# Optimization experiments

Hardware: AMD Instinct MI355X
Metric: run time of the kernel (lower is better)

The kernel has to match this reference:

```python
import jax, jax.numpy as jnp
import numpy as np

N_NODES = 50000
NNZ = 1_600_000
D_FEAT = 256


def setup_inputs() -> dict:
    key = jax.random.key(0)
    k_x, k_v, k_r, k_c = jax.random.split(key, 4)
    x = jax.random.normal(k_x, (N_NODES, D_FEAT), dtype=jnp.float32)
    # learned per-nonzero values; torch init uses std = 1/sqrt(mean col degree)
    std = 1.0 / np.sqrt(NNZ / N_NODES)
    values = jax.random.normal(k_v, (NNZ,), dtype=jnp.float32) * std
    row = jax.random.randint(k_r, (NNZ,), 0, N_NODES, dtype=jnp.int64)
    col = jax.random.randint(k_c, (NNZ,), 0, N_NODES, dtype=jnp.int64)
    return {"x": x, "values": values, "row": row, "col": col}


def reference(x, values, row, col):
    # Math identical to matmul(to_dense(coo(row, col, values)), x):
    # out[r] = sum over edges e with row[e]==r of values[e] * x[col[e]]
    msgs = values[:, None] * x[col]            # [nnz, F]
    out = jax.ops.segment_sum(msgs, row, num_segments=N_NODES)  # [N, F]
    return out
```

## Files before the change

kernel.cpp:

```cpp
#include <hip/hip_runtime.h>
#include <hip/hip_bf16.h>


#define FEAT 256
#define CAP 128
#define SCAN_CHUNK 2048

static __device__ __forceinline__ unsigned short f2bf(float f) {
    unsigned int u = __float_as_uint(f);
    u += 0x7FFF + ((u >> 16) & 1);
    return (unsigned short)(u >> 16);
}
static __device__ __forceinline__ float bf2f(unsigned short h) {
    return __uint_as_float(((unsigned int)h) << 16);
}


__global__ __launch_bounds__(256) void zero_convx_kernel(const float4* __restrict__ x4,
                                                         ushort4* __restrict__ xh,
                                                         int* __restrict__ deg,
                                                         int n, int n4) {
    const int stride = gridDim.x * blockDim.x;
    const int tid = blockIdx.x * blockDim.x + threadIdx.x;
    for (int i = tid; i < n; i += stride) deg[i] = 0;
    for (int i = tid; i < n4; i += stride) {
        float4 v = x4[i];
        ushort4 o;
        o.x = f2bf(v.x); o.y = f2bf(v.y); o.z = f2bf(v.z); o.w = f2bf(v.w);
        xh[i] = o;
    }
}

__global__ __launch_bounds__(256) void bucket_scatter_kernel(const int* __restrict__ row,
                                                             const int* __restrict__ col,
                                                             const float* __restrict__ vals,
                                                             int* __restrict__ deg,
                                                             int2* __restrict__ pack,
                                                             int nnz) {
    const int stride = gridDim.x * blockDim.x;
    for (int e = blockIdx.x * blockDim.x + threadIdx.x; e < nnz; e += stride) {
        int r = row[e];
        int pos = atomicAdd(&deg[r], 1);
        if (pos < CAP) pack[(size_t)r * CAP + pos] = make_int2(col[e], __float_as_int(vals[e]));
    }
}

__global__ __launch_bounds__(256) void spmm_bucket_kernel(const ushort4* __restrict__ xh,
                                                          const int2* __restrict__ pack,
                                                          const int* __restrict__ deg,
                                                          float* __restrict__ out, int n) {
    const int wave = threadIdx.x >> 6;
    const int lane = threadIdx.x & 63;
    const int r = blockIdx.x * 4 + wave;
    if (r >= n) return;
    int d = deg[r]; if (d > CAP) d = CAP;
    const int2* __restrict__ bucket = pack + (size_t)r * CAP;
    float4 acc = make_float4(0.f, 0.f, 0.f, 0.f);
    for (int k0 = 0; k0 < d; k0 += 64) {
        int cnt = d - k0; if (cnt > 64) cnt = 64;
        float myv = 0.f; int myc = 0;
        if (lane < cnt) {
            int2 pr = bucket[k0 + lane];
            myc = pr.x;
            myv = __int_as_float(pr.y);
        }
        for (int j = 0; j < cnt; ++j) {
            float v = __shfl(myv, j);
            int   c = __shfl(myc, j);
            ushort4 h = xh[c * 64 + lane];
            acc.x += v * bf2f(h.x);
            acc.y += v * bf2f(h.y);
            acc.z += v * bf2f(h.z);
            acc.w += v * bf2f(h.w);
        }
    }
    ((float4*)out)[r * 64 + lane] = acc;
}


__global__ void convx_kernel(const float4* __restrict__ x, ushort4* __restrict__ xh, int n4) {
    int stride = gridDim.x * blockDim.x;
    for (int i = blockIdx.x * blockDim.x + threadIdx.x; i < n4; i += stride) {
        float4 v = x[i];
        ushort4 o;
        o.x = f2bf(v.x); o.y = f2bf(v.y); o.z = f2bf(v.z); o.w = f2bf(v.w);
        xh[i] = o;
    }
}

__global__ void hist_rank_kernel(const int* __restrict__ row, int* __restrict__ deg,
                                 int* __restrict__ rank, int nnz) {
    int stride = gridDim.x * blockDim.x;
    for (int e = blockIdx.x * blockDim.x + threadIdx.x; e < nnz; e += stride) {
        rank[e] = atomicAdd(&deg[row[e]], 1);
    }
}

__global__ __launch_bounds__(256) void scan_chunks_kernel(const int* __restrict__ deg,
                                                          int* __restrict__ rowstart,
                                                          int* __restrict__ partials, int n) {
    __shared__ int s[256];
    const int tid = threadIdx.x;
    const int base = blockIdx.x * SCAN_CHUNK + tid * 8;
    int items[8];
    int sum = 0;
    #pragma unroll
    for (int j = 0; j < 8; ++j) {
        int v = (base + j < n) ? deg[base + j] : 0;
        items[j] = sum;
        sum += v;
    }
    s[tid] = sum;
    __syncthreads();
    for (int off = 1; off < 256; off <<= 1) {
        int t = (tid >= off) ? s[tid - off] : 0;
        __syncthreads();
        s[tid] += t;
        __syncthreads();
    }
    int thread_prefix = s[tid] - sum;
    if (tid == 255) partials[blockIdx.x] = s[255];
    #pragma unroll
    for (int j = 0; j < 8; ++j) {
        if (base + j < n) rowstart[base + j] = items[j] + thread_prefix;
    }
}

__global__ __launch_bounds__(256) void finalize_scan_kernel(int* __restrict__ rowstart,
                                                            const int* __restrict__ partials,
                                                            int n, int nnz) {
    __shared__ int sprefix;
    const int cb = (int)((blockIdx.x * 256u) / SCAN_CHUNK);
    if (threadIdx.x < 64) {
        int v = (threadIdx.x < cb) ? partials[threadIdx.x] : 0;
        #pragma unroll
        for (int off = 32; off; off >>= 1) v += __shfl_down(v, off);
        if (threadIdx.x == 0) sprefix = v;
    }
    __syncthreads();
    int i = blockIdx.x * 256 + threadIdx.x;
    if (i < n) rowstart[i] += sprefix;
    if (i == 0) rowstart[n] = nnz;
}

__global__ void scatter_pack_kernel(const int* __restrict__ row, const int* __restrict__ rank,
                                    const int* __restrict__ col, const float* __restrict__ vals,
                                    const int* __restrict__ rowstart, int2* __restrict__ pack,
                                    int nnz) {
    int stride = gridDim.x * blockDim.x;
    for (int e = blockIdx.x * blockDim.x + threadIdx.x; e < nnz; e += stride) {
        int p = rowstart[row[e]] + rank[e];
        pack[p] = make_int2(col[e], __float_as_int(vals[e]));
    }
}

__global__ __launch_bounds__(256) void spmm_bf16_kernel(const ushort4* __restrict__ xh,
                                                        const int2* __restrict__ pack,
                                                        const int* __restrict__ rowstart,
                                                        float* __restrict__ out, int n) {
    const int wave = threadIdx.x >> 6;
    const int lane = threadIdx.x & 63;
    const int r = blockIdx.x * 4 + wave;
    if (r >= n) return;
    const int s = rowstart[r];
    const int e = rowstart[r + 1];
    float4 acc = make_float4(0.f, 0.f, 0.f, 0.f);
    for (int k0 = s; k0 < e; k0 += 64) {
        int cnt = e - k0; if (cnt > 64) cnt = 64;
        float myv = 0.f; int myc = 0;
        if (lane < cnt) {
            int2 pr = pack[k0 + lane];
            myc = pr.x;
            myv = __int_as_float(pr.y);
        }
        for (int j = 0; j < cnt; ++j) {
            float v = __shfl(myv, j);
            int   c = __shfl(myc, j);
            ushort4 h = xh[c * 64 + lane];
            acc.x += v * bf2f(h.x);
            acc.y += v * bf2f(h.y);
            acc.z += v * bf2f(h.z);
            acc.w += v * bf2f(h.w);
        }
    }
    ((float4*)out)[r * 64 + lane] = acc;
}


extern "C" void kernel_launch(void* const* d_in, const int* in_sizes, int n_in,
                              void* d_out, int out_size, void* d_ws, size_t ws_size,
                              hipStream_t stream) {
    const float* x    = (const float*)d_in[0];
    const float* vals = (const float*)d_in[1];
    const int*   row  = (const int*)d_in[2];
    const int*   col  = (const int*)d_in[3];
    float* out = (float*)d_out;

    const int nnz = in_sizes[1];
    const int n   = out_size / FEAT;
    const int nb  = (n + SCAN_CHUNK - 1) / SCAN_CHUNK;

    {
        char* p0 = (char*)d_ws;
        char* p = p0;
        int* deg = (int*)p;            p += (size_t)n * 4;
        p = (char*)((((size_t)p) + 15) & ~(size_t)15);
        int2* pack = (int2*)p;         p += (size_t)n * CAP * 8;
        ushort4* xh = (ushort4*)p;     p += (size_t)n * FEAT * 2;
        const size_t need = (size_t)(p - p0);
        if (ws_size >= need) {
            const int n4 = n * (FEAT / 4);
            zero_convx_kernel<<<2048, 256, 0, stream>>>((const float4*)x, xh, deg, n, n4);
            bucket_scatter_kernel<<<2048, 256, 0, stream>>>(row, col, vals, deg, pack, nnz);
            spmm_bucket_kernel<<<(n + 3) / 4, 256, 0, stream>>>(xh, pack, deg, out, n);
            return;
        }
    }

    {
        char* p0 = (char*)d_ws;
        char* p = p0;
        int* deg      = (int*)p; p += (size_t)n * 4;
        int* rowstart = (int*)p; p += (size_t)(n + 1) * 4;
        int* partials = (int*)p; p += 64 * 4;
        int* rank     = (int*)p; p += (size_t)nnz * 4;
        p = (char*)((((size_t)p) + 7) & ~(size_t)7);
        int2* pack    = (int2*)p; p += (size_t)nnz * 8;
        unsigned short* xh = (unsigned short*)p; p += (size_t)n * FEAT * 2;
        const size_t need = (size_t)(p - p0);
        if (ws_size >= need) {
            hipMemsetAsync(deg, 0, (size_t)n * 4, stream);
            hist_rank_kernel<<<2048, 256, 0, stream>>>(row, deg, rank, nnz);
            convx_kernel<<<2048, 256, 0, stream>>>((const float4*)x, (ushort4*)xh, n * (FEAT / 4));
            scan_chunks_kernel<<<nb, 256, 0, stream>>>(deg, rowstart, partials, n);
            finalize_scan_kernel<<<(n + 255) / 256, 256, 0, stream>>>(rowstart, partials, n, nnz);
            scatter_pack_kernel<<<2048, 256, 0, stream>>>(row, rank, col, vals, rowstart, pack, nnz);
            spmm_bf16_kernel<<<(n + 3) / 4, 256, 0, stream>>>((const ushort4*)xh, pack, rowstart, out, n);
        }
    }
}
```

Before: 331.2 us.

## Fuse bf16 conversion with bucket scatter and batch gathers in SpMM inner loop

Merges the x-to-bf16 conversion and the row-bucket scatter into one prep kernel, with deg zeroed by a memset beforehand. This removes a launch and lets conversion traffic overlap with the atomic scatter. In the SpMM kernel the per-neighbor shuffles become readlane broadcasts, and eight gathers are issued before the FMAs to expose more memory-level parallelism. Bucket entries are packed as 64-bit words and read with nontemporal loads; the cost is higher register use per wave.

```diff
diff --git a/kernel.cpp b/kernel.cpp
--- a/kernel.cpp
+++ b/kernel.cpp
@@ -16,37 +16,35 @@
 }
 
 
-__global__ __launch_bounds__(256) void zero_convx_kernel(const float4* __restrict__ x4,
-                                                         ushort4* __restrict__ xh,
-                                                         int* __restrict__ deg,
-                                                         int n, int n4) {
+__global__ __launch_bounds__(256) void prep_kernel(const float4* __restrict__ x4,
+                                                   ushort4* __restrict__ xh,
+                                                   const int* __restrict__ row,
+                                                   const int* __restrict__ col,
+                                                   const float* __restrict__ vals,
+                                                   int* __restrict__ deg,
+                                                   unsigned long long* __restrict__ pack,
+                                                   int n4, int nnz) {
     const int stride = gridDim.x * blockDim.x;
     const int tid = blockIdx.x * blockDim.x + threadIdx.x;
-    for (int i = tid; i < n; i += stride) deg[i] = 0;
     for (int i = tid; i < n4; i += stride) {
         float4 v = x4[i];
         ushort4 o;
         o.x = f2bf(v.x); o.y = f2bf(v.y); o.z = f2bf(v.z); o.w = f2bf(v.w);
         xh[i] = o;
     }
-}
-
-__global__ __launch_bounds__(256) void bucket_scatter_kernel(const int* __restrict__ row,
-                                                             const int* __restrict__ col,
-                                                             const float* __restrict__ vals,
-                                                             int* __restrict__ deg,
-                                                             int2* __restrict__ pack,
-                                                             int nnz) {
-    const int stride = gridDim.x * blockDim.x;
-    for (int e = blockIdx.x * blockDim.x + threadIdx.x; e < nnz; e += stride) {
+    for (int e = tid; e < nnz; e += stride) {
         int r = row[e];
         int pos = atomicAdd(&deg[r], 1);
-        if (pos < CAP) pack[(size_t)r * CAP + pos] = make_int2(col[e], __float_as_int(vals[e]));
+        if (pos < CAP) {
+            unsigned long long pr = ((unsigned long long)(unsigned int)__float_as_uint(vals[e]) << 32)
+                                  | (unsigned int)col[e];
+            pack[(size_t)r * CAP + pos] = pr;
+        }
     }
 }
 
 __global__ __launch_bounds__(256) void spmm_bucket_kernel(const ushort4* __restrict__ xh,
-                                                          const int2* __restrict__ pack,
+                                                          const unsigned long long* __restrict__ pack,
                                                           const int* __restrict__ deg,
                                                           float* __restrict__ out, int n) {
     const int wave = threadIdx.x >> 6;
@@ -54,24 +52,33 @@
     const int r = blockIdx.x * 4 + wave;
     if (r >= n) return;
     int d = deg[r]; if (d > CAP) d = CAP;
-    const int2* __restrict__ bucket = pack + (size_t)r * CAP;
+    const unsigned long long* __restrict__ bucket = pack + (size_t)r * CAP;
     float4 acc = make_float4(0.f, 0.f, 0.f, 0.f);
     for (int k0 = 0; k0 < d; k0 += 64) {
         int cnt = d - k0; if (cnt > 64) cnt = 64;
         float myv = 0.f; int myc = 0;
         if (lane < cnt) {
-            int2 pr = bucket[k0 + lane];
-            myc = pr.x;
-            myv = __int_as_float(pr.y);
-        }
-        for (int j = 0; j < cnt; ++j) {
-            float v = __shfl(myv, j);
-            int   c = __shfl(myc, j);
-            ushort4 h = xh[c * 64 + lane];
-            acc.x += v * bf2f(h.x);
-            acc.y += v * bf2f(h.y);
-            acc.z += v * bf2f(h.z);
-            acc.w += v * bf2f(h.w);
+            unsigned long long pr = __builtin_nontemporal_load(&bucket[k0 + lane]);
+            myc = (int)(unsigned int)(pr & 0xFFFFFFFFu);
+            myv = __uint_as_float((unsigned int)(pr >> 32));
+        }
+        for (int j = 0; j < cnt; j += 8) {
+            ushort4 h[8];
+            float vv[8];
+            #pragma unroll
+            for (int k = 0; k < 8; ++k) {
+                int sidx = j + k; if (sidx > 63) sidx = 63;
+                int cc = __builtin_amdgcn_readlane(myc, sidx);
+                vv[k] = __uint_as_float(__builtin_amdgcn_readlane(__float_as_uint(myv), sidx));
+                h[k] = xh[(size_t)cc * 64 + lane];
+            }
+            #pragma unroll
+            for (int k = 0; k < 8; ++k) {
+                acc.x += vv[k] * bf2f(h[k].x);
+                acc.y += vv[k] * bf2f(h[k].y);
+                acc.z += vv[k] * bf2f(h[k].z);
+                acc.w += vv[k] * bf2f(h[k].w);
+            }
         }
     }
     ((float4*)out)[r * 64 + lane] = acc;
@@ -205,13 +212,14 @@
         char* p = p0;
         int* deg = (int*)p;            p += (size_t)n * 4;
         p = (char*)((((size_t)p) + 15) & ~(size_t)15);
-        int2* pack = (int2*)p;         p += (size_t)n * CAP * 8;
+        unsigned long long* pack = (unsigned long long*)p; p += (size_t)n * CAP * 8;
         ushort4* xh = (ushort4*)p;     p += (size_t)n * FEAT * 2;
         const size_t need = (size_t)(p - p0);
         if (ws_size >= need) {
             const int n4 = n * (FEAT / 4);
-            zero_convx_kernel<<<2048, 256, 0, stream>>>((const float4*)x, xh, deg, n, n4);
-            bucket_scatter_kernel<<<2048, 256, 0, stream>>>(row, col, vals, deg, pack, nnz);
+            (void)hipMemsetAsync(deg, 0, (size_t)n * 4, stream);
+            prep_kernel<<<2048, 256, 0, stream>>>((const float4*)x, xh, row, col, vals,
+                                                  deg, pack, n4, nnz);
             spmm_bucket_kernel<<<(n + 3) / 4, 256, 0, stream>>>(xh, pack, deg, out, n);
             return;
         }
@@ -229,7 +237,7 @@
         unsigned short* xh = (unsigned short*)p; p += (size_t)n * FEAT * 2;
         const size_t need = (size_t)(p - p0);
         if (ws_size >= need) {
-            hipMemsetAsync(deg, 0, (size_t)n * 4, stream);
+            (void)hipMemsetAsync(deg, 0, (size_t)n * 4, stream);
             hist_rank_kernel<<<2048, 256, 0, stream>>>(row, deg, rank, nnz);
             convx_kernel<<<2048, 256, 0, stream>>>((const float4*)x, (ushort4*)xh, n * (FEAT / 4));
             scan_chunks_kernel<<<nb, 256, 0, stream>>>(deg, rowstart, partials, n);
```

After: 318.6 us. 1.04x faster.
